# Optimization experiments

Measured on AMD Instinct MI355X. Metric: run time of the kernel, lower is better.

## Reference

```python
import jax, jax.numpy as jnp
import numpy as np

B, Lq, Dlen, P = 32, 32, 4096, 16
V, D, H = 50257, 2048, 2048


def setup_inputs() -> dict:
    key = jax.random.key(0)
    k = jax.random.split(key, 7)
    queries = jax.random.randint(k[0], (B, Lq), 0, V)
    query_lengths = jax.random.randint(k[1], (B,), 4, Lq + 1).astype(jnp.int32)
    docs = jax.random.randint(k[2], (B, Dlen), 0, V)
    # passage lengths in [32, 255]; cumsum <= 16*255 < Dlen so all passages fit
    passage_lengths = jax.random.randint(k[3], (B, P), 32, 256).astype(jnp.int32)
    emb = jax.random.normal(k[4], (V, D), jnp.float32) * 0.02
    W = jax.random.normal(k[5], (H, D), jnp.float32) * (1.0 / np.sqrt(D))
    b = jnp.zeros((H,), jnp.float32)
    return dict(queries=queries, query_lengths=query_lengths, docs=docs,
                passage_lengths=passage_lengths, emb=emb, W=W, b=b)


def reference(queries, query_lengths, docs, passage_lengths, emb, W, b):
    # --- encode queries: masked mean of token embeddings, then linear ---
    q_emb = emb[queries]  # [B,Lq,D]
    q_mask = (jnp.arange(Lq)[None, :] < query_lengths[:, None]).astype(q_emb.dtype)
    q_rep = jnp.einsum('bl,bld->bd', q_mask, q_emb) / query_lengths[:, None].astype(q_emb.dtype)
    q_enc = q_rep @ W.T + b  # [B,H]

    # --- split docs into passages via segment ids from cumulative lengths ---
    d_emb = emb[docs]  # [B,T,D]
    cum = jnp.cumsum(passage_lengths, axis=1)  # [B,P]
    t = jnp.arange(Dlen)
    seg = jnp.sum(t[None, :, None] >= cum[:, None, :], axis=-1)  # [B,T], token -> passage id
    valid = t[None, :] < cum[:, -1:]  # tokens past total doc length are padding
    onehot = ((seg[:, :, None] == jnp.arange(P)[None, None, :]) & valid[:, :, None]).astype(d_emb.dtype)
    sums = jnp.einsum('btp,btd->bpd', onehot, d_emb)  # per-passage embedding sums
    denom = jnp.maximum(passage_lengths, 1).astype(d_emb.dtype)[:, :, None]
    p_rep = sums / denom  # [B,P,D] masked mean
    p_enc = p_rep @ W.T + b  # [B,P,H]

    # --- dot-product scoring (dropout = identity in eval mode) ---
    scores = jnp.einsum('bh,bph->bp', q_enc, p_enc)
    return scores * (passage_lengths > 0).astype(scores.dtype)
```

## Files before the change

### kernel.cpp

```cpp
#include <hip/hip_runtime.h>

#define B 32
#define LQ 32
#define DLEN 4096
#define P 16
#define D 2048
#define H 2048
#define NC 32
#define HC 32
#define HB 4

__global__ __launch_bounds__(256) void zero_kernel(float* __restrict__ v,
                                                   float* __restrict__ sacc) {
  const int i = blockIdx.x * 256 + threadIdx.x;
  if (i < B * D) v[i] = 0.f;
  if (i < B * P) sacc[i] = 0.f;
}

__global__ __launch_bounds__(256) void qrep_kernel(
    const int* __restrict__ queries, const int* __restrict__ qlen,
    const float* __restrict__ emb, float* __restrict__ q_rep) {
  __shared__ int stok[LQ];
  const int b   = blockIdx.x;
  const int len = qlen[b];
  if (threadIdx.x < len) stok[threadIdx.x] = queries[b * LQ + threadIdx.x];
  __syncthreads();

  float4 a0 = make_float4(0.f, 0.f, 0.f, 0.f);
  float4 a1 = make_float4(0.f, 0.f, 0.f, 0.f);
  for (int t = 0; t < len; ++t) {
    const float4* r = (const float4*)(emb + (size_t)stok[t] * D);
    const float4 x = r[threadIdx.x];
    const float4 y = r[threadIdx.x + 256];
    a0.x += x.x; a0.y += x.y; a0.z += x.z; a0.w += x.w;
    a1.x += y.x; a1.y += y.y; a1.z += y.z; a1.w += y.w;
  }
  const float inv = 1.0f / (float)len;
  float4* o = (float4*)(q_rep + (size_t)b * D);
  o[threadIdx.x]       = make_float4(a0.x*inv, a0.y*inv, a0.z*inv, a0.w*inv);
  o[threadIdx.x + 256] = make_float4(a1.x*inv, a1.y*inv, a1.z*inv, a1.w*inv);
}

__global__ __launch_bounds__(256) void qenc_kernel(
    const float* __restrict__ q_rep, const float* __restrict__ W,
    const float* __restrict__ bias, float* __restrict__ q_enc) {
  const int h0 = blockIdx.x * HB;
  __shared__ float4 wsh[HB][D / 4];
  for (int i = threadIdx.x; i < HB * (D / 4); i += 256) {
    const int r = i / (D / 4), c = i % (D / 4);
    wsh[r][c] = ((const float4*)(W + (size_t)(h0 + r) * D))[c];
  }
  __syncthreads();

  const int lane = threadIdx.x & 63, wid = threadIdx.x >> 6;
  for (int b = wid; b < B; b += 4) {
    const float4* q4 = (const float4*)(q_rep + (size_t)b * D);
    float s[HB] = {0.f, 0.f, 0.f, 0.f};
#pragma unroll
    for (int j = 0; j < 8; ++j) {
      const float4 q = q4[j * 64 + lane];
#pragma unroll
      for (int r = 0; r < HB; ++r) {
        const float4 w = wsh[r][j * 64 + lane];
        s[r] += w.x * q.x + w.y * q.y + w.z * q.z + w.w * q.w;
      }
    }
#pragma unroll
    for (int r = 0; r < HB; ++r) {
      float t = s[r];
#pragma unroll
      for (int off = 32; off; off >>= 1) t += __shfl_down(t, off, 64);
      if (lane == 0) q_enc[b * H + h0 + r] = t + bias[h0 + r];
    }
  }
}

__global__ __launch_bounds__(256) void v_kernel(
    const float* __restrict__ q_enc, const float* __restrict__ W,
    float* __restrict__ v) {
  const int d  = blockIdx.x * 256 + threadIdx.x;
  const int h0 = blockIdx.y * HC;

  __shared__ float qe[HC][B];
  for (int i = threadIdx.x; i < HC * B; i += 256)
    qe[i >> 5][i & 31] = q_enc[(i & 31) * H + h0 + (i >> 5)];
  __syncthreads();

  float acc[B];
#pragma unroll
  for (int b = 0; b < B; ++b) acc[b] = 0.f;

#pragma unroll 4
  for (int hh = 0; hh < HC; ++hh) {
    const float w = W[(size_t)(h0 + hh) * D + d];
#pragma unroll
    for (int b = 0; b < B; ++b) acc[b] += w * qe[hh][b];
  }
#pragma unroll
  for (int b = 0; b < B; ++b) atomicAdd(&v[b * D + d], acc[b]);
}

__global__ __launch_bounds__(256) void docscore_kernel(
    const int* __restrict__ docs, const int* __restrict__ plen,
    const float* __restrict__ emb, const float* __restrict__ v,
    float* __restrict__ sacc) {
  const int b = blockIdx.y;
  __shared__ float4 vsh[D / 4];
  __shared__ int    cum[P];
  __shared__ int    stok[128];
  __shared__ unsigned char sp[128];
  __shared__ float  wacc[4][P];

  vsh[threadIdx.x]       = ((const float4*)(v + (size_t)b * D))[threadIdx.x];
  vsh[threadIdx.x + 256] = ((const float4*)(v + (size_t)b * D))[threadIdx.x + 256];
  if (threadIdx.x == 0) {
    int s = 0;
#pragma unroll
    for (int i = 0; i < P; ++i) { s += plen[b * P + i]; cum[i] = s; }
  }
  if (threadIdx.x < 4 * P) wacc[threadIdx.x >> 4][threadIdx.x & 15] = 0.f;
  __syncthreads();

  const int tot = cum[P - 1];
  const int per = (tot + NC - 1) / NC;
  const int t0  = blockIdx.x * per;
  const int t1  = (t0 + per < tot) ? (t0 + per) : tot;
  const int cnt = t1 - t0;

  for (int i = threadIdx.x; i < cnt; i += 256) {
    const int t = t0 + i;
    stok[i] = docs[b * DLEN + t];
    int p = 0;
#pragma unroll
    for (int j = 0; j < P; ++j) p += (t >= cum[j]) ? 1 : 0;
    sp[i] = (unsigned char)p;
  }
  __syncthreads();

  const int lane = threadIdx.x & 63, wid = threadIdx.x >> 6;
  for (int i = wid; i < cnt; i += 4) {
    const float4* e4 = (const float4*)(emb + (size_t)stok[i] * D);
    float s = 0.f;
#pragma unroll
    for (int j = 0; j < 8; ++j) {
      const float4 e = e4[j * 64 + lane];
      const float4 w = vsh[j * 64 + lane];
      s += e.x * w.x + e.y * w.y + e.z * w.z + e.w * w.w;
    }
#pragma unroll
    for (int off = 32; off; off >>= 1) s += __shfl_down(s, off, 64);
    if (lane == 0) wacc[wid][sp[i]] += s;
  }
  __syncthreads();

  if (threadIdx.x < P) {
    const float r = wacc[0][threadIdx.x] + wacc[1][threadIdx.x] +
                    wacc[2][threadIdx.x] + wacc[3][threadIdx.x];
    atomicAdd(&sacc[b * P + threadIdx.x], r);
  }
}

__global__ __launch_bounds__(256) void final_kernel(
    const float* __restrict__ q_enc, const float* __restrict__ bias,
    const float* __restrict__ sacc, const int* __restrict__ plen,
    float* __restrict__ out) {
  const int b = blockIdx.x;
  float s = 0.f;
#pragma unroll
  for (int k = 0; k < 8; ++k) {
    const int c = k * 256 + threadIdx.x;
    s += q_enc[b * H + c] * bias[c];
  }
#pragma unroll
  for (int off = 32; off; off >>= 1) s += __shfl_down(s, off, 64);

  __shared__ float red[4];
  __shared__ float qb;
  const int lane = threadIdx.x & 63, wid = threadIdx.x >> 6;
  if (lane == 0) red[wid] = s;
  __syncthreads();
  if (threadIdx.x == 0) qb = red[0] + red[1] + red[2] + red[3];
  __syncthreads();

  if (threadIdx.x < P) {
    const int l = plen[b * P + threadIdx.x];
    const float val = sacc[b * P + threadIdx.x] / (float)(l > 0 ? l : 1) + qb;
    out[b * P + threadIdx.x] = (l > 0) ? val : 0.f;
  }
}

extern "C" void kernel_launch(void* const* d_in, const int* in_sizes, int n_in,
                              void* d_out, int out_size, void* d_ws, size_t ws_size,
                              hipStream_t stream) {
  const int*   queries = (const int*)d_in[0];
  const int*   qlen    = (const int*)d_in[1];
  const int*   docs    = (const int*)d_in[2];
  const int*   plen    = (const int*)d_in[3];
  const float* emb     = (const float*)d_in[4];
  const float* W       = (const float*)d_in[5];
  const float* bias    = (const float*)d_in[6];
  float*       out     = (float*)d_out;

  float* v     = (float*)d_ws;
  float* sacc  = v + B * D;
  float* q_rep = sacc + B * P;
  float* q_enc = q_rep + B * D;

  zero_kernel<<<(B * D + 255) / 256, 256, 0, stream>>>(v, sacc);
  qrep_kernel<<<B, 256, 0, stream>>>(queries, qlen, emb, q_rep);
  qenc_kernel<<<H / HB, 256, 0, stream>>>(q_rep, W, bias, q_enc);
  dim3 vgrid(D / 256, H / HC);
  v_kernel<<<vgrid, 256, 0, stream>>>(q_enc, W, v);
  dim3 dgrid(NC, B);
  docscore_kernel<<<dgrid, 256, 0, stream>>>(docs, plen, emb, v, sacc);
  final_kernel<<<B, 256, 0, stream>>>(q_enc, bias, sacc, plen, out);
}
```

Before: 609.6 us.

## Compute passage embedding sums first, then score against projected query vector

Replaces the per-token dot-product doc scoring with a psum kernel that accumulates per-passage embedding sums via atomics. A small score kernel then dots each sum with v. The q·bias term moves into qenc as an atomic accumulation, and HC doubles in v_kernel. The intent is to take the doc embedding gather off the critical path after v and use cheaper accumulation, at the cost of many global atomics on a 4 MB p_sum buffer and a larger zeroing pass.

```diff
diff --git a/kernel.cpp b/kernel.cpp
--- a/kernel.cpp
+++ b/kernel.cpp
@@ -7,14 +7,70 @@
 #define D 2048
 #define H 2048
 #define NC 32
-#define HC 32
+#define HC 64
 #define HB 4
 
-__global__ __launch_bounds__(256) void zero_kernel(float* __restrict__ v,
-                                                   float* __restrict__ sacc) {
+#define ZERO_N (B * P * D + B * D + B)
+
+__global__ __launch_bounds__(256) void zero_kernel(float* __restrict__ ws) {
   const int i = blockIdx.x * 256 + threadIdx.x;
-  if (i < B * D) v[i] = 0.f;
-  if (i < B * P) sacc[i] = 0.f;
+  if (i < ZERO_N) ws[i] = 0.f;
+}
+
+__global__ __launch_bounds__(256) void psum_kernel(
+    const int* __restrict__ docs, const int* __restrict__ plen,
+    const float* __restrict__ emb, float* __restrict__ p_sum) {
+  const int b = blockIdx.y;
+  __shared__ int cum[P];
+  __shared__ int stok[128];
+
+  if (threadIdx.x == 0) {
+    int s = 0;
+#pragma unroll
+    for (int i = 0; i < P; ++i) { s += plen[b * P + i]; cum[i] = s; }
+  }
+  __syncthreads();
+
+  const int tot = cum[P - 1];
+  const int per = (tot + NC - 1) / NC;
+  const int t0  = blockIdx.x * per;
+  const int t1  = (t0 + per < tot) ? (t0 + per) : tot;
+  if (t0 >= t1) return;
+
+  for (int i = threadIdx.x; i < t1 - t0; i += 256)
+    stok[i] = docs[b * DLEN + t0 + i];
+  __syncthreads();
+
+  int p = 0;
+#pragma unroll
+  for (int j = 0; j < P; ++j) p += (cum[j] <= t0) ? 1 : 0;
+
+  const int tid = threadIdx.x;
+  int segStart = t0;
+  while (segStart < t1) {
+    const int segEnd = (cum[p] < t1) ? cum[p] : t1;
+    float4 a0 = make_float4(0.f, 0.f, 0.f, 0.f);
+    float4 a1 = make_float4(0.f, 0.f, 0.f, 0.f);
+#pragma unroll 2
+    for (int t = segStart; t < segEnd; ++t) {
+      const float4* r = (const float4*)(emb + (size_t)stok[t - t0] * D);
+      const float4 x = r[tid];
+      const float4 y = r[tid + 256];
+      a0.x += x.x; a0.y += x.y; a0.z += x.z; a0.w += x.w;
+      a1.x += y.x; a1.y += y.y; a1.z += y.z; a1.w += y.w;
+    }
+    float* dst = p_sum + (size_t)(b * P + p) * D;
+    atomicAdd(&dst[tid * 4 + 0], a0.x);
+    atomicAdd(&dst[tid * 4 + 1], a0.y);
+    atomicAdd(&dst[tid * 4 + 2], a0.z);
+    atomicAdd(&dst[tid * 4 + 3], a0.w);
+    atomicAdd(&dst[1024 + tid * 4 + 0], a1.x);
+    atomicAdd(&dst[1024 + tid * 4 + 1], a1.y);
+    atomicAdd(&dst[1024 + tid * 4 + 2], a1.z);
+    atomicAdd(&dst[1024 + tid * 4 + 3], a1.w);
+    segStart = segEnd;
+    ++p;
+  }
 }
 
 __global__ __launch_bounds__(256) void qrep_kernel(
@@ -35,7 +91,7 @@
     a0.x += x.x; a0.y += x.y; a0.z += x.z; a0.w += x.w;
     a1.x += y.x; a1.y += y.y; a1.z += y.z; a1.w += y.w;
   }
-  const float inv = 1.0f / (float)len;
+  const float inv = 1.0f / (float)(len > 0 ? len : 1);
   float4* o = (float4*)(q_rep + (size_t)b * D);
   o[threadIdx.x]       = make_float4(a0.x*inv, a0.y*inv, a0.z*inv, a0.w*inv);
   o[threadIdx.x + 256] = make_float4(a1.x*inv, a1.y*inv, a1.z*inv, a1.w*inv);
@@ -43,7 +99,8 @@
 
 __global__ __launch_bounds__(256) void qenc_kernel(
     const float* __restrict__ q_rep, const float* __restrict__ W,
-    const float* __restrict__ bias, float* __restrict__ q_enc) {
+    const float* __restrict__ bias, float* __restrict__ q_enc,
+    float* __restrict__ qb) {
   const int h0 = blockIdx.x * HB;
   __shared__ float4 wsh[HB][D / 4];
   for (int i = threadIdx.x; i < HB * (D / 4); i += 256) {
@@ -65,13 +122,20 @@
         s[r] += w.x * q.x + w.y * q.y + w.z * q.z + w.w * q.w;
       }
     }
+    float qbp = 0.f;
 #pragma unroll
     for (int r = 0; r < HB; ++r) {
       float t = s[r];
 #pragma unroll
       for (int off = 32; off; off >>= 1) t += __shfl_down(t, off, 64);
-      if (lane == 0) q_enc[b * H + h0 + r] = t + bias[h0 + r];
+      if (lane == 0) {
+        const float bh  = bias[h0 + r];
+        const float val = t + bh;
+        q_enc[b * H + h0 + r] = val;
+        qbp += val * bh;
+      }
     }
+    if (lane == 0) atomicAdd(&qb[b], qbp);
   }
 }
 
@@ -100,92 +164,35 @@
   for (int b = 0; b < B; ++b) atomicAdd(&v[b * D + d], acc[b]);
 }
 
-__global__ __launch_bounds__(256) void docscore_kernel(
-    const int* __restrict__ docs, const int* __restrict__ plen,
-    const float* __restrict__ emb, const float* __restrict__ v,
-    float* __restrict__ sacc) {
-  const int b = blockIdx.y;
-  __shared__ float4 vsh[D / 4];
-  __shared__ int    cum[P];
-  __shared__ int    stok[128];
-  __shared__ unsigned char sp[128];
-  __shared__ float  wacc[4][P];
-
-  vsh[threadIdx.x]       = ((const float4*)(v + (size_t)b * D))[threadIdx.x];
-  vsh[threadIdx.x + 256] = ((const float4*)(v + (size_t)b * D))[threadIdx.x + 256];
-  if (threadIdx.x == 0) {
-    int s = 0;
-#pragma unroll
-    for (int i = 0; i < P; ++i) { s += plen[b * P + i]; cum[i] = s; }
-  }
-  if (threadIdx.x < 4 * P) wacc[threadIdx.x >> 4][threadIdx.x & 15] = 0.f;
-  __syncthreads();
-
-  const int tot = cum[P - 1];
-  const int per = (tot + NC - 1) / NC;
-  const int t0  = blockIdx.x * per;
-  const int t1  = (t0 + per < tot) ? (t0 + per) : tot;
-  const int cnt = t1 - t0;
-
-  for (int i = threadIdx.x; i < cnt; i += 256) {
-    const int t = t0 + i;
-    stok[i] = docs[b * DLEN + t];
-    int p = 0;
-#pragma unroll
-    for (int j = 0; j < P; ++j) p += (t >= cum[j]) ? 1 : 0;
-    sp[i] = (unsigned char)p;
-  }
-  __syncthreads();
-
-  const int lane = threadIdx.x & 63, wid = threadIdx.x >> 6;
-  for (int i = wid; i < cnt; i += 4) {
-    const float4* e4 = (const float4*)(emb + (size_t)stok[i] * D);
-    float s = 0.f;
-#pragma unroll
-    for (int j = 0; j < 8; ++j) {
-      const float4 e = e4[j * 64 + lane];
-      const float4 w = vsh[j * 64 + lane];
-      s += e.x * w.x + e.y * w.y + e.z * w.z + e.w * w.w;
-    }
-#pragma unroll
-    for (int off = 32; off; off >>= 1) s += __shfl_down(s, off, 64);
-    if (lane == 0) wacc[wid][sp[i]] += s;
-  }
-  __syncthreads();
-
-  if (threadIdx.x < P) {
-    const float r = wacc[0][threadIdx.x] + wacc[1][threadIdx.x] +
-                    wacc[2][threadIdx.x] + wacc[3][threadIdx.x];
-    atomicAdd(&sacc[b * P + threadIdx.x], r);
-  }
-}
-
-__global__ __launch_bounds__(256) void final_kernel(
-    const float* __restrict__ q_enc, const float* __restrict__ bias,
-    const float* __restrict__ sacc, const int* __restrict__ plen,
+__global__ __launch_bounds__(256) void score_kernel(
+    const float* __restrict__ v, const float* __restrict__ p_sum,
+    const float* __restrict__ qb, const int* __restrict__ plen,
     float* __restrict__ out) {
-  const int b = blockIdx.x;
+  const int bp = blockIdx.x;
+  const int b  = bp >> 4;
+
+  const float4* v4 = (const float4*)(v + (size_t)b * D);
+  const float4* s4 = (const float4*)(p_sum + (size_t)bp * D);
   float s = 0.f;
 #pragma unroll
-  for (int k = 0; k < 8; ++k) {
+  for (int k = 0; k < 2; ++k) {
     const int c = k * 256 + threadIdx.x;
-    s += q_enc[b * H + c] * bias[c];
+    const float4 a = v4[c];
+    const float4 x = s4[c];
+    s += a.x * x.x + a.y * x.y + a.z * x.z + a.w * x.w;
   }
 #pragma unroll
   for (int off = 32; off; off >>= 1) s += __shfl_down(s, off, 64);
 
   __shared__ float red[4];
-  __shared__ float qb;
   const int lane = threadIdx.x & 63, wid = threadIdx.x >> 6;
   if (lane == 0) red[wid] = s;
   __syncthreads();
-  if (threadIdx.x == 0) qb = red[0] + red[1] + red[2] + red[3];
-  __syncthreads();
-
-  if (threadIdx.x < P) {
-    const int l = plen[b * P + threadIdx.x];
-    const float val = sacc[b * P + threadIdx.x] / (float)(l > 0 ? l : 1) + qb;
-    out[b * P + threadIdx.x] = (l > 0) ? val : 0.f;
+  if (threadIdx.x == 0) {
+    const int   l   = plen[bp];
+    const float tot = red[0] + red[1] + red[2] + red[3];
+    const float val = tot / (float)(l > 0 ? l : 1) + qb[b];
+    out[bp] = (l > 0) ? val : 0.f;
   }
 }
 
@@ -201,17 +208,19 @@
   const float* bias    = (const float*)d_in[6];
   float*       out     = (float*)d_out;
 
-  float* v     = (float*)d_ws;
-  float* sacc  = v + B * D;
-  float* q_rep = sacc + B * P;
+  float* ws    = (float*)d_ws;
+  float* p_sum = ws;
+  float* v     = p_sum + (size_t)B * P * D;
+  float* qb    = v + B * D;
+  float* q_rep = qb + B;
   float* q_enc = q_rep + B * D;
 
-  zero_kernel<<<(B * D + 255) / 256, 256, 0, stream>>>(v, sacc);
+  zero_kernel<<<(ZERO_N + 255) / 256, 256, 0, stream>>>(ws);
+  dim3 pgrid(NC, B);
+  psum_kernel<<<pgrid, 256, 0, stream>>>(docs, plen, emb, p_sum);
   qrep_kernel<<<B, 256, 0, stream>>>(queries, qlen, emb, q_rep);
-  qenc_kernel<<<H / HB, 256, 0, stream>>>(q_rep, W, bias, q_enc);
+  qenc_kernel<<<H / HB, 256, 0, stream>>>(q_rep, W, bias, q_enc, qb);
   dim3 vgrid(D / 256, H / HC);
   v_kernel<<<vgrid, 256, 0, stream>>>(q_enc, W, v);
-  dim3 dgrid(NC, B);
-  docscore_kernel<<<dgrid, 256, 0, stream>>>(docs, plen, emb, v, sacc);
-  final_kernel<<<B, 256, 0, stream>>>(q_enc, bias, sacc, plen, out);
-}
+  score_kernel<<<B * P, 256, 0, stream>>>(v, p_sum, qb, plen, out);
+}
```

Result: slower. 787.7 us (+29.2%).
